# Performance work log

Measured on AMD Instinct MI355X. Metric: run time of the kernel, lower is better.

The kernel has to match this reference:

```python
import math
import jax, jax.numpy as jnp
import numpy as np

EMBED_DIM = 512
NUM_HEADS = 8
EDGE_VOC = 16
EDGE_PAD = 0
L, B = 512, 16


def setup_inputs() -> dict:
    key = jax.random.key(0)
    ks = jax.random.split(key, 8)
    x = jax.random.normal(ks[0], (L, B, EMBED_DIM), dtype=jnp.float32)
    edge = jax.random.randint(ks[1], (B, L, L), 0, EDGE_VOC, dtype=jnp.int32)
    key_padding_mask = jnp.zeros((B, L), dtype=bool)
    # causal additive mask, as from nn.Transformer.generate_square_subsequent_mask
    attn_mask = jnp.where(jnp.triu(jnp.ones((L, L), bool), k=1), -jnp.inf, 0.0).astype(jnp.float32)
    s = 1.0 / math.sqrt(EMBED_DIM)
    in_proj_w = jax.random.uniform(ks[2], (3 * EMBED_DIM, EMBED_DIM), jnp.float32, -s, s)
    in_proj_b = jnp.zeros((3 * EMBED_DIM,), jnp.float32)
    out_proj_w = jax.random.uniform(ks[3], (EMBED_DIM, EMBED_DIM), jnp.float32, -s, s)
    out_proj_b = jnp.zeros((EMBED_DIM,), jnp.float32)
    edge_emb = jax.random.normal(ks[4], (EDGE_VOC, NUM_HEADS), dtype=jnp.float32)
    edge_emb = edge_emb.at[EDGE_PAD].set(0.0)  # padding_idx row zeroed
    return {"x": x, "edge": edge, "key_padding_mask": key_padding_mask,
            "attn_mask": attn_mask, "in_proj_w": in_proj_w, "in_proj_b": in_proj_b,
            "out_proj_w": out_proj_w, "out_proj_b": out_proj_b, "edge_emb": edge_emb}


def reference(x, edge, key_padding_mask, attn_mask,
              in_proj_w, in_proj_b, out_proj_w, out_proj_b, edge_emb):
    length, bsz, embed_dim = x.shape
    H = edge_emb.shape[1]
    hd = embed_dim // H
    qkv = x @ in_proj_w.T + in_proj_b                       # (L, B, 3E)
    q, k, v = jnp.split(qkv, 3, axis=-1)
    # (L, B*H, hd) -> (B*H, L, hd)
    q = q.reshape(length, bsz * H, hd).transpose(1, 0, 2)
    k = k.reshape(length, bsz * H, hd).transpose(1, 0, 2)
    v = v.reshape(length, bsz * H, hd).transpose(1, 0, 2)
    # combine attn_mask with key padding
    mask = attn_mask[None]                                   # (1, L, L)
    kpm = jnp.broadcast_to(key_padding_mask[:, None, None, :],
                           (bsz, H, 1, length)).reshape(bsz * H, 1, length)
    mask = jnp.where(kpm, -jnp.inf, mask)                    # (B*H, 1/L, L)
    # edge bias: (B, L, L, H) -> (B*H, L, L)
    ebias = edge_emb[edge].transpose(0, 3, 1, 2).reshape(bsz * H, length, length)
    q = q / math.sqrt(hd)
    scores = jnp.einsum('bqd,bkd->bqk', q, k) + mask + ebias
    attn = jax.nn.softmax(scores, axis=-1)
    out = jnp.einsum('bqk,bkd->bqd', attn, v)                # (B*H, L, hd)
    out = out.transpose(1, 0, 2).reshape(length, bsz, embed_dim)
    return out @ out_proj_w.T + out_proj_b
```

## Files before the change

### kernel.cpp

```cpp
#include <hip/hip_runtime.h>
#include <hip/hip_bf16.h>


typedef __attribute__((ext_vector_type(8))) short bf16x8;
typedef __attribute__((ext_vector_type(4))) float f32x4;
typedef __attribute__((ext_vector_type(4))) int i32x4;

#define LOG2E 1.44269504088896340736f
#define QK_SCALE 0.18033688011112042f

__device__ inline void gll16(const void* g, const void* l) {
  __builtin_amdgcn_global_load_lds(
      (const __attribute__((address_space(1))) unsigned int*)g,
      (__attribute__((address_space(3))) unsigned int*)l, 16, 0, 0);
}

__device__ inline short f2bf(float x) {
  __hip_bfloat16 t = __float2bfloat16(x);
  return *reinterpret_cast<short*>(&t);
}

__device__ inline void cstore(__hip_bfloat16* C, size_t idx, float v) {
  C[idx] = __float2bfloat16(v);
}
__device__ inline void cstore(float* C, size_t idx, float v) { C[idx] = v; }

__global__ void cvt3(const float* __restrict__ x, const float* __restrict__ w1,
                     const float* __restrict__ w2, const int* __restrict__ edge,
                     __hip_bfloat16* __restrict__ xb,
                     __hip_bfloat16* __restrict__ w1b,
                     __hip_bfloat16* __restrict__ w2b,
                     unsigned char* __restrict__ epk) {
  const int blk = blockIdx.x;
  const int tid = threadIdx.x;
  if (blk >= 2560) {
    __shared__ unsigned char Ls[4 * 512];
    const int pblk = blk - 2560;
    const int b = pblk >> 7;
    const int q0 = (pblk & 127) * 4;
    const int row = tid >> 6, lk = tid & 63;
    const int k0 = lk * 8;
    const int* src = edge + ((size_t)(b * 512 + q0 + row)) * 512 + k0;
    const i32x4 a = *(const i32x4*)src;
    const i32x4 b4 = *(const i32x4*)(src + 4);
    const unsigned int lo =
        (unsigned)a[0] | ((unsigned)a[1] << 8) | ((unsigned)a[2] << 16) |
        ((unsigned)a[3] << 24);
    const unsigned int hi =
        (unsigned)b4[0] | ((unsigned)b4[1] << 8) | ((unsigned)b4[2] << 16) |
        ((unsigned)b4[3] << 24);
    const int kt = k0 >> 6, kk = k0 & 63;
    const int mt = kk >> 4, quad = (kk >> 2) & 3;
    const int doff = row * 512 + kt * 64 + quad * 16 + mt * 4;
    *(unsigned int*)&Ls[doff] = lo;
    *(unsigned int*)&Ls[doff + 16] = hi;
    __syncthreads();
    const int okt = tid >> 5, rowi = (tid >> 3) & 3, off8 = (tid & 7) * 8;
    const unsigned long long v =
        *(const unsigned long long*)&Ls[rowi * 512 + okt * 64 + off8];
    *(unsigned long long*)&epk[(((size_t)(b * 8 + okt) * 512) + q0 + rowi) *
                                   64 +
                               off8] = v;
    return;
  }
  const float* src;
  __hip_bfloat16* dst;
  int off;
  if (blk < 2048)      { src = x;  dst = xb;  off = blk; }
  else if (blk < 2432) { src = w1; dst = w1b; off = blk - 2048; }
  else                 { src = w2; dst = w2b; off = blk - 2432; }
  const int i = (off * 256 + tid) * 8;
  const float4 a = *(const float4*)(src + i);
  const float4 b = *(const float4*)(src + i + 4);
  bf16x8 r;
  r[0] = f2bf(a.x); r[1] = f2bf(a.y); r[2] = f2bf(a.z); r[3] = f2bf(a.w);
  r[4] = f2bf(b.x); r[5] = f2bf(b.y); r[6] = f2bf(b.z); r[7] = f2bf(b.w);
  *(bf16x8*)(dst + i) = r;
}

template <int MT, int RB, typename TC, bool QS = false, bool BROW = false>
__global__ __launch_bounds__(256, RB) void gemm_bt(
    const __hip_bfloat16* __restrict__ A,
    const __hip_bfloat16* __restrict__ W,
    const float* __restrict__ bias,
    TC* __restrict__ C, int N, int K) {
  constexpr int MI = MT / 32;
  __shared__ short As[MT * 32];
  __shared__ short Ws[128 * 32];
  const int tid = threadIdx.x;
  const int wave = tid >> 6, lane = tid & 63;
  const int c = lane & 15, quad = lane >> 4;
  const int nb = N >> 7;
  const int bx = blockIdx.x % nb, by = blockIdx.x / nb;
  const int m0 = by * MT, n0 = bx << 7;
  const int wm = wave >> 1, wn = wave & 1;

  f32x4 acc[MI][4] = {};
  const int ar = lane >> 2;
  const int ak = (lane & 3) * 8;

  for (int k0 = 0; k0 < K; k0 += 32) {
    __syncthreads();
#pragma unroll
    for (int i = 0; i < MT / 64; i++) {
      const int r0 = i * 64 + wave * 16;
      gll16(A + (size_t)(m0 + r0 + ar) * K + k0 + ak, &As[r0 * 32]);
    }
#pragma unroll
    for (int i = 0; i < 2; i++) {
      const int r0 = i * 64 + wave * 16;
      gll16(W + (size_t)(n0 + r0 + ar) * K + k0 + ak, &Ws[r0 * 32]);
    }
    __syncthreads();
    bf16x8 af[MI], bfr[4];
#pragma unroll
    for (int i = 0; i < MI; i++)
      af[i] = *(const bf16x8*)&As[(wm * (MT / 2) + i * 16 + c) * 32 + quad * 8];
#pragma unroll
    for (int j = 0; j < 4; j++)
      bfr[j] = *(const bf16x8*)&Ws[(wn * 64 + j * 16 + c) * 32 + quad * 8];
#pragma unroll
    for (int i = 0; i < MI; i++)
#pragma unroll
      for (int j = 0; j < 4; j++)
        acc[i][j] = __builtin_amdgcn_mfma_f32_16x16x32_bf16(af[i], bfr[j],
                                                            acc[i][j], 0, 0, 0);
  }
#pragma unroll
  for (int j = 0; j < 4; j++) {
    const int col = n0 + wn * 64 + j * 16 + c;
    const float bv = bias[col];
#pragma unroll
    for (int i = 0; i < MI; i++) {
      const int row = m0 + wm * (MT / 2) + i * 16 + quad * 4;
#pragma unroll
      for (int r = 0; r < 4; r++) {
        float v = acc[i][j][r] + bv;
        if constexpr (QS) {
          if (col < 512) v *= QK_SCALE;
        }
        int orow = row + r;
        if constexpr (BROW) orow = ((orow & 15) << 9) | (orow >> 4);
        cstore(C, (size_t)orow * N + col, v);
      }
    }
  }
}

__global__ __launch_bounds__(256, 4) void attn_kernel(
    const __hip_bfloat16* __restrict__ qkv,
    const unsigned char* __restrict__ epk,
    const float* __restrict__ edge_emb,
    __hip_bfloat16* __restrict__ attn_out) {
  __shared__ short Ks[64 * 72];
  __shared__ short Vt[64 * 72];
  __shared__ short Ps[4][16 * 72];
  __shared__ float eeS[16];

  const int tid = threadIdx.x;
  const int wave = tid >> 6, lane = tid & 63;
  const int c = lane & 15, quad = lane >> 4;
  const int i = blockIdx.x;
  constexpr int pi[8] = {0, 7, 1, 6, 2, 5, 3, 4};
  const int xcd = i & 7;
  const int j = i >> 3;
  const int qb = pi[(j + (j >> 5)) & 7];
  const int h = (j >> 3) & 7;
  const int b = xcd + ((j >> 6) << 3);
  const int colq = h * 64;

  if (tid < 16) eeS[tid] = (edge_emb[tid * 8 + h] - 16.0f) * LOG2E;

  const int q_g = (qb << 6) + wave * 16 + c;
  bf16x8 qf0, qf1;
  {
    const __hip_bfloat16* qp_ = qkv + (size_t)(b * 512 + q_g) * 1536 + colq;
    qf0 = *(const bf16x8*)(qp_ + quad * 8);
    qf1 = *(const bf16x8*)(qp_ + 32 + quad * 8);
  }
  float lsum = 0.f;
  f32x4 o[4] = {};
  const unsigned char* eb =
      epk + (((size_t)(b * 8) * 512 + q_g) << 6) + (quad << 4);

  const int r2 = tid >> 3;
  const int cc = (tid & 7) * 8;
  const int kcol0 = ((r2 << 1) & 7) | (((r2 >> 2) ^ (cc >> 3)) << 3);
  const size_t sbase0 = (size_t)(b * 512 + r2 * 2) * 1536 + colq + cc;
  bf16x8 kreg[2], vreg[2];
  kreg[0] = *(const bf16x8*)(qkv + sbase0 + 512);
  vreg[0] = *(const bf16x8*)(qkv + sbase0 + 1024);
  kreg[1] = *(const bf16x8*)(qkv + sbase0 + 1536 + 512);
  vreg[1] = *(const bf16x8*)(qkv + sbase0 + 1536 + 1024);

  __syncthreads();

  const int nkt = qb + 1;
  for (int kt = 0; kt < nkt; kt++) {
    const bool last = (kt == qb);
    const int mtmax = last ? (wave + 1) : 4;
    if (kt) __syncthreads();
    *(bf16x8*)&Ks[(r2 * 2) * 72 + cc] = kreg[0];
    *(bf16x8*)&Ks[(r2 * 2 + 1) * 72 + cc] = kreg[1];
#pragma unroll
    for (int j2 = 0; j2 < 8; j2++) {
      short2 p;
      p.x = vreg[0][j2];
      p.y = vreg[1][j2];
      *(short2*)&Vt[(cc + j2) * 72 + kcol0] = p;
    }
    if (kt + 1 < nkt) {
      const size_t nb_ = sbase0 + (size_t)(kt + 1) * 64 * 1536;
      kreg[0] = *(const bf16x8*)(qkv + nb_ + 512);
      vreg[0] = *(const bf16x8*)(qkv + nb_ + 1024);
      kreg[1] = *(const bf16x8*)(qkv + nb_ + 1536 + 512);
      vreg[1] = *(const bf16x8*)(qkv + nb_ + 1536 + 1024);
    }
    const i32x4 e16 = *(const i32x4*)(eb + ((size_t)kt << 15));
    __syncthreads();

    f32x4 st[4];
    __builtin_amdgcn_s_setprio(1);
#pragma unroll
    for (int mt = 0; mt < 4; mt++) {
      if (mt >= mtmax) continue;
      const unsigned int w = (unsigned int)e16[mt];
      f32x4 z;
#pragma unroll
      for (int r = 0; r < 4; r++) z[r] = eeS[(w >> (8 * r)) & 15];
      const bf16x8 ka = *(const bf16x8*)&Ks[(mt * 16 + c) * 72 + quad * 8];
      const bf16x8 kb = *(const bf16x8*)&Ks[(mt * 16 + c) * 72 + 32 + quad * 8];
      z = __builtin_amdgcn_mfma_f32_16x16x32_bf16(ka, qf0, z, 0, 0, 0);
      st[mt] = __builtin_amdgcn_mfma_f32_16x16x32_bf16(kb, qf1, z, 0, 0, 0);
    }
    __builtin_amdgcn_s_setprio(0);

    float rs[4] = {0.f, 0.f, 0.f, 0.f};
#pragma unroll
    for (int mt = 0; mt < 4; mt++) {
      short4 pk = {0, 0, 0, 0};
      if (mt < mtmax) {
        if (last && mt == wave) {
#pragma unroll
          for (int r = 0; r < 4; r++) {
            const float p = (quad * 4 + r <= c) ? exp2f(st[mt][r]) : 0.0f;
            rs[r] += p;
            ((short*)&pk)[r] = f2bf(p);
          }
        } else {
#pragma unroll
          for (int r = 0; r < 4; r++) {
            const float p = exp2f(st[mt][r]);
            rs[r] += p;
            ((short*)&pk)[r] = f2bf(p);
          }
        }
      }
      *(short4*)&Ps[wave][c * 72 + mt * 16 + quad * 4] = pk;
    }
    lsum += (rs[0] + rs[1]) + (rs[2] + rs[3]);

    const bool skip_hi = last && (wave < 2);
    const bf16x8 pa0 = *(const bf16x8*)&Ps[wave][c * 72 + quad * 8];
    bf16x8 pa1;
    if (!skip_hi) pa1 = *(const bf16x8*)&Ps[wave][c * 72 + 32 + quad * 8];
    __builtin_amdgcn_s_setprio(1);
#pragma unroll
    for (int nt = 0; nt < 4; nt++) {
      const int n = nt * 16 + c;
      const bf16x8 vb0 = *(const bf16x8*)&Vt[n * 72 + ((quad ^ (n >> 3)) << 3)];
      o[nt] = __builtin_amdgcn_mfma_f32_16x16x32_bf16(pa0, vb0, o[nt], 0, 0, 0);
      if (!skip_hi) {
        const bf16x8 vb1 =
            *(const bf16x8*)&Vt[n * 72 + (((4 + quad) ^ (n >> 3)) << 3)];
        o[nt] = __builtin_amdgcn_mfma_f32_16x16x32_bf16(pa1, vb1, o[nt], 0, 0, 0);
      }
    }
    __builtin_amdgcn_s_setprio(0);
  }

  float l = lsum;
  l += __shfl_xor(l, 16);
  l += __shfl_xor(l, 32);
  float lr[4];
#pragma unroll
  for (int r = 0; r < 4; r++) lr[r] = __shfl(l, quad * 4 + r, 16);
  const int qrow0 = (qb << 6) + wave * 16 + quad * 4;
#pragma unroll
  for (int nt = 0; nt < 4; nt++)
#pragma unroll
    for (int r = 0; r < 4; r++)
      attn_out[(size_t)((qrow0 + r) * 16 + b) * 512 + colq + nt * 16 + c] =
          __float2bfloat16(o[nt][r] / lr[r]);
}

extern "C" void kernel_launch(void* const* d_in, const int* in_sizes, int n_in,
                              void* d_out, int out_size, void* d_ws, size_t ws_size,
                              hipStream_t stream) {
  const float* x    = (const float*)d_in[0];
  const int* edge   = (const int*)d_in[1];
  const float* ipw  = (const float*)d_in[4];
  const float* ipb  = (const float*)d_in[5];
  const float* opw  = (const float*)d_in[6];
  const float* opb  = (const float*)d_in[7];
  const float* eemb = (const float*)d_in[8];
  float* out = (float*)d_out;

  __hip_bfloat16* qkv  = (__hip_bfloat16*)d_ws;
  __hip_bfloat16* attn = qkv + (size_t)8192 * 1536;
  __hip_bfloat16* xb   = attn + (size_t)8192 * 512;
  __hip_bfloat16* w1b  = xb + (size_t)8192 * 512;
  __hip_bfloat16* w2b  = w1b + (size_t)1536 * 512;
  unsigned char* epk = (unsigned char*)(w2b + (size_t)512 * 512);

  cvt3<<<4608, 256, 0, stream>>>(x, ipw, opw, edge, xb, w1b, w2b, epk);
  gemm_bt<128, 3, __hip_bfloat16, true, true>
      <<<768, 256, 0, stream>>>(xb, w1b, ipb, qkv, 1536, 512);
  attn_kernel<<<1024, 256, 0, stream>>>(qkv, epk, eemb, attn);
  gemm_bt<64, 2, float>
      <<<512, 256, 0, stream>>>(attn, w2b, opb, out, 512, 512);
}
```

Before: 148.6 us.

## Load K fragments directly from global into registers, bypassing LDS staging

Drops the shared-memory K tile. Each wave now loads its K MFMA operand fragments straight from global memory into registers and prefetches the next tile's K fragments and edge bytes right after the QK MFMAs. This removes the LDS writes and reads for K and frees LDS. In exchange each wave issues its own redundant, less-coalesced global loads of K, and register pressure rises with eight extra bf16x8 fragments held per thread.

Measured after the change: 153.7 us. +3.4%, slower.

```diff
diff --git a/kernel.cpp b/kernel.cpp
--- a/kernel.cpp
+++ b/kernel.cpp
@@ -152,7 +152,6 @@
     const unsigned char* __restrict__ epk,
     const float* __restrict__ edge_emb,
     __hip_bfloat16* __restrict__ attn_out) {
-  __shared__ short Ks[64 * 72];
   __shared__ short Vt[64 * 72];
   __shared__ short Ps[4][16 * 72];
   __shared__ float eeS[16];
@@ -168,6 +167,7 @@
   const int h = (j >> 3) & 7;
   const int b = xcd + ((j >> 6) << 3);
   const int colq = h * 64;
+  const int nkt = qb + 1;
 
   if (tid < 16) eeS[tid] = (edge_emb[tid * 8 + h] - 16.0f) * LOG2E;
 
@@ -182,26 +182,36 @@
   f32x4 o[4] = {};
   const unsigned char* eb =
       epk + (((size_t)(b * 8) * 512 + q_g) << 6) + (quad << 4);
+  const __hip_bfloat16* kfb_base =
+      qkv + (size_t)(b * 512 + c) * 1536 + colq + 512 + quad * 8;
 
   const int r2 = tid >> 3;
   const int cc = (tid & 7) * 8;
   const int kcol0 = ((r2 << 1) & 7) | (((r2 >> 2) ^ (cc >> 3)) << 3);
   const size_t sbase0 = (size_t)(b * 512 + r2 * 2) * 1536 + colq + cc;
-  bf16x8 kreg[2], vreg[2];
-  kreg[0] = *(const bf16x8*)(qkv + sbase0 + 512);
+  bf16x8 vreg[2];
   vreg[0] = *(const bf16x8*)(qkv + sbase0 + 1024);
-  kreg[1] = *(const bf16x8*)(qkv + sbase0 + 1536 + 512);
   vreg[1] = *(const bf16x8*)(qkv + sbase0 + 1536 + 1024);
 
+  bf16x8 kfa[4], kfb[4];
+  {
+    const int m0max = (0 == qb) ? (wave + 1) : 4;
+#pragma unroll
+    for (int mt = 0; mt < 4; mt++)
+      if (mt < m0max) {
+        const __hip_bfloat16* p_ = kfb_base + (size_t)(mt * 16) * 1536;
+        kfa[mt] = *(const bf16x8*)p_;
+        kfb[mt] = *(const bf16x8*)(p_ + 32);
+      }
+  }
+  i32x4 e16 = *(const i32x4*)eb;
+
   __syncthreads();
 
-  const int nkt = qb + 1;
   for (int kt = 0; kt < nkt; kt++) {
     const bool last = (kt == qb);
     const int mtmax = last ? (wave + 1) : 4;
     if (kt) __syncthreads();
-    *(bf16x8*)&Ks[(r2 * 2) * 72 + cc] = kreg[0];
-    *(bf16x8*)&Ks[(r2 * 2 + 1) * 72 + cc] = kreg[1];
 #pragma unroll
     for (int j2 = 0; j2 < 8; j2++) {
       short2 p;
@@ -211,12 +221,9 @@
     }
     if (kt + 1 < nkt) {
       const size_t nb_ = sbase0 + (size_t)(kt + 1) * 64 * 1536;
-      kreg[0] = *(const bf16x8*)(qkv + nb_ + 512);
       vreg[0] = *(const bf16x8*)(qkv + nb_ + 1024);
-      kreg[1] = *(const bf16x8*)(qkv + nb_ + 1536 + 512);
       vreg[1] = *(const bf16x8*)(qkv + nb_ + 1536 + 1024);
     }
-    const i32x4 e16 = *(const i32x4*)(eb + ((size_t)kt << 15));
     __syncthreads();
 
     f32x4 st[4];
@@ -228,12 +235,23 @@
       f32x4 z;
 #pragma unroll
       for (int r = 0; r < 4; r++) z[r] = eeS[(w >> (8 * r)) & 15];
-      const bf16x8 ka = *(const bf16x8*)&Ks[(mt * 16 + c) * 72 + quad * 8];
-      const bf16x8 kb = *(const bf16x8*)&Ks[(mt * 16 + c) * 72 + 32 + quad * 8];
-      z = __builtin_amdgcn_mfma_f32_16x16x32_bf16(ka, qf0, z, 0, 0, 0);
-      st[mt] = __builtin_amdgcn_mfma_f32_16x16x32_bf16(kb, qf1, z, 0, 0, 0);
+      z = __builtin_amdgcn_mfma_f32_16x16x32_bf16(kfa[mt], qf0, z, 0, 0, 0);
+      st[mt] = __builtin_amdgcn_mfma_f32_16x16x32_bf16(kfb[mt], qf1, z, 0, 0, 0);
     }
     __builtin_amdgcn_s_setprio(0);
+
+    if (kt + 1 < nkt) {
+      const int nmt = (kt + 1 == qb) ? (wave + 1) : 4;
+      const __hip_bfloat16* nb2 = kfb_base + (size_t)((kt + 1) * 64) * 1536;
+#pragma unroll
+      for (int mt = 0; mt < 4; mt++)
+        if (mt < nmt) {
+          const __hip_bfloat16* p_ = nb2 + (size_t)(mt * 16) * 1536;
+          kfa[mt] = *(const bf16x8*)p_;
+          kfb[mt] = *(const bf16x8*)(p_ + 32);
+        }
+      e16 = *(const i32x4*)(eb + ((size_t)(kt + 1) << 15));
+    }
 
     float rs[4] = {0.f, 0.f, 0.f, 0.f};
 #pragma unroll
```

## Transpose softmax probabilities in registers via permlane swaps instead of LDS

Applied to the files above, without the earlier changes.

Removes the per-wave LDS staging buffer used to reshape the P tile from the MFMA output layout into the A-operand layout. P values are packed to bf16 with v_cvt_pk_bf16_f32 and redistributed across lanes with v_permlane32_swap and v_permlane16_swap. This is meant to drop LDS writes and reads plus their latency from the inner loop and to free shared memory. It depends on the lane-permutation mapping being exactly correct for the 16x16x32 operand layout, and the inline asm may limit compiler scheduling.

Measured after the change: 148.3 us. About the same (-0.2%).

```diff
diff --git a/kernel.cpp b/kernel.cpp
--- a/kernel.cpp
+++ b/kernel.cpp
@@ -5,6 +5,7 @@
 typedef __attribute__((ext_vector_type(8))) short bf16x8;
 typedef __attribute__((ext_vector_type(4))) float f32x4;
 typedef __attribute__((ext_vector_type(4))) int i32x4;
+typedef __attribute__((ext_vector_type(4))) unsigned int u32x4;
 
 #define LOG2E 1.44269504088896340736f
 #define QK_SCALE 0.18033688011112042f
@@ -154,7 +155,6 @@
     __hip_bfloat16* __restrict__ attn_out) {
   __shared__ short Ks[64 * 72];
   __shared__ short Vt[64 * 72];
-  __shared__ short Ps[4][16 * 72];
   __shared__ float eeS[16];
 
   const int tid = threadIdx.x;
@@ -235,35 +235,61 @@
     }
     __builtin_amdgcn_s_setprio(0);
 
+    unsigned int wp[4][2];
     float rs[4] = {0.f, 0.f, 0.f, 0.f};
 #pragma unroll
     for (int mt = 0; mt < 4; mt++) {
-      short4 pk = {0, 0, 0, 0};
       if (mt < mtmax) {
+        float pv[4];
         if (last && mt == wave) {
 #pragma unroll
           for (int r = 0; r < 4; r++) {
-            const float p = (quad * 4 + r <= c) ? exp2f(st[mt][r]) : 0.0f;
-            rs[r] += p;
-            ((short*)&pk)[r] = f2bf(p);
+            pv[r] = (quad * 4 + r <= c) ? exp2f(st[mt][r]) : 0.0f;
+            rs[r] += pv[r];
           }
         } else {
 #pragma unroll
           for (int r = 0; r < 4; r++) {
-            const float p = exp2f(st[mt][r]);
-            rs[r] += p;
-            ((short*)&pk)[r] = f2bf(p);
+            pv[r] = exp2f(st[mt][r]);
+            rs[r] += pv[r];
           }
         }
+        asm("v_cvt_pk_bf16_f32 %0, %1, %2"
+            : "=v"(wp[mt][0]) : "v"(pv[0]), "v"(pv[1]));
+        asm("v_cvt_pk_bf16_f32 %0, %1, %2"
+            : "=v"(wp[mt][1]) : "v"(pv[2]), "v"(pv[3]));
+      } else {
+        wp[mt][0] = 0u;
+        wp[mt][1] = 0u;
       }
-      *(short4*)&Ps[wave][c * 72 + mt * 16 + quad * 4] = pk;
     }
     lsum += (rs[0] + rs[1]) + (rs[2] + rs[3]);
 
     const bool skip_hi = last && (wave < 2);
-    const bf16x8 pa0 = *(const bf16x8*)&Ps[wave][c * 72 + quad * 8];
+    u32x4 paw;
+    {
+      unsigned int a0 = wp[0][0], b0 = wp[1][0];
+      asm("v_permlane32_swap_b32 %0, %1" : "+v"(a0), "+v"(b0));
+      asm("v_permlane16_swap_b32 %0, %1" : "+v"(a0), "+v"(b0));
+      unsigned int a1 = wp[0][1], b1 = wp[1][1];
+      asm("v_permlane32_swap_b32 %0, %1" : "+v"(a1), "+v"(b1));
+      asm("v_permlane16_swap_b32 %0, %1" : "+v"(a1), "+v"(b1));
+      paw[0] = a0; paw[1] = a1; paw[2] = b0; paw[3] = b1;
+    }
+    const bf16x8 pa0 = *(const bf16x8*)&paw;
     bf16x8 pa1;
-    if (!skip_hi) pa1 = *(const bf16x8*)&Ps[wave][c * 72 + 32 + quad * 8];
+    if (!skip_hi) {
+      u32x4 pbw;
+      unsigned int a0 = wp[2][0], b0 = wp[3][0];
+      asm("v_permlane32_swap_b32 %0, %1" : "+v"(a0), "+v"(b0));
+      asm("v_permlane16_swap_b32 %0, %1" : "+v"(a0), "+v"(b0));
+      unsigned int a1 = wp[2][1], b1 = wp[3][1];
+      asm("v_permlane32_swap_b32 %0, %1" : "+v"(a1), "+v"(b1));
+      asm("v_permlane16_swap_b32 %0, %1" : "+v"(a1), "+v"(b1));
+      pbw[0] = a0; pbw[1] = a1; pbw[2] = b0; pbw[3] = b1;
+      pa1 = *(const bf16x8*)&pbw;
+    }
+
     __builtin_amdgcn_s_setprio(1);
 #pragma unroll
     for (int nt = 0; nt < 4; nt++) {
```
